# Kernel tuning notes

Measured on AMD Instinct MI355X. Metric: run time of the kernel, lower is better.

Reference implementation:

```python
import jax, jax.numpy as jnp
import numpy as np

TEMPERATURE = 1.0
MAX_ITERS = 10
EPSILON = 1e-4
N, D, K = 131072, 64, 64


def setup_inputs() -> dict:
    key = jax.random.key(0)
    k1, k2 = jax.random.split(key)
    weights = jax.random.normal(k1, (N, D), dtype=jnp.float32)
    init_clusters = jax.random.normal(k2, (K, D), dtype=jnp.float32)
    return {"weights": weights, "init_clusters": init_clusters}


def _dkm(weights, init_clusters):
    n, d = weights.shape
    k = init_clusters.shape[0]
    w_sq = jnp.sum(weights * weights, axis=1, keepdims=True)  # [N,1]

    def step(carry, _):
        clusters, attn_prev, done = carry
        # Euclidean cdist via the expansion ||w||^2 + ||c||^2 - 2 w.c
        c_sq = jnp.sum(clusters * clusters, axis=1)               # [K]
        d2 = w_sq + c_sq[None, :] - 2.0 * (weights @ clusters.T)  # [N,K]
        dist = jnp.sqrt(jnp.maximum(d2, 0.0))
        attn = jax.nn.softmax(-dist / TEMPERATURE, axis=-1)        # [N,K]
        new_clusters = (attn.T @ weights) / jnp.sum(attn, axis=0)[:, None]  # [K,D]
        converged = jnp.linalg.norm(clusters - new_clusters) <= EPSILON
        # Torch breaks BEFORE assigning new_clusters; emulate with a done flag.
        clusters_next = jnp.where(done | converged, clusters, new_clusters)
        attn_next = jnp.where(done, attn_prev, attn)
        return (clusters_next, attn_next, done | converged), None

    init = (init_clusters, jnp.zeros((n, k), weights.dtype), jnp.array(False))
    (clusters, attn, _), _ = jax.lax.scan(step, init, None, length=MAX_ITERS)
    compressed = attn @ clusters  # [N,D]
    return compressed, clusters, attn


def reference(weights, init_clusters):
    return _dkm(weights, init_clusters)
```

## Files before the change

kernel.cpp:

```cpp
#include <hip/hip_runtime.h>
#include <math.h>
#include <stdint.h>

#define N_ROWS 131072
#define DIM 64
#define KC 64
#define NBLK 512
#define ROWS_PB 256

typedef __attribute__((ext_vector_type(8))) short short8;
typedef __attribute__((ext_vector_type(8))) unsigned short ushort8;
typedef __attribute__((ext_vector_type(16))) float float16;
typedef __attribute__((ext_vector_type(2))) unsigned long long ulong2v;

#define PARTIAL_OFF 0u
#define SUMA_OFF    2097152u
#define WSQ_OFF     2129920u
#define NEWC_OFF    2260992u
#define NORM_BYTE_OFF (2265088ull * 4ull)

__device__ __forceinline__ uint32_t rne16(float a) {
  uint32_t u = __float_as_uint(a);
  return (u + 0x7fffu + ((u >> 16) & 1u)) >> 16;
}

__device__ __forceinline__ uint32_t pack_bf16(float a, float b) {
  return rne16(a) | (rne16(b) << 16);
}

__device__ __forceinline__ void split2(float a, float b, uint32_t& hi, uint32_t& lo) {
  uint32_t ha = rne16(a), hb = rne16(b);
  hi = ha | (hb << 16);
  float la = a - __uint_as_float(ha << 16);
  float lb = b - __uint_as_float(hb << 16);
  lo = pack_bf16(la, lb);
}

__global__ __launch_bounds__(256) void prep_kernel(const float* __restrict__ W,
                                                   unsigned short* WS,
                                                   float* __restrict__ wsq) {
  const int t = threadIdx.x;
  const int r = blockIdx.x * 256 + t;
  const float4* p = (const float4*)(W + (size_t)r * DIM);
  uint32_t* hi = (uint32_t*)(WS + (size_t)r * 128);
  uint32_t* lo = hi + 32;
  float s = 0.f;
#pragma unroll
  for (int c = 0; c < 16; ++c) {
    float4 v = p[c];
    s += v.x * v.x + v.y * v.y + v.z * v.z + v.w * v.w;
    uint32_t h0, h1, l0, l1;
    split2(v.x, v.y, h0, l0);
    split2(v.z, v.w, h1, l1);
    hi[c * 2] = h0; hi[c * 2 + 1] = h1;
    lo[c * 2] = l0; lo[c * 2 + 1] = l1;
  }
  wsq[r] = s;
}

__global__ __launch_bounds__(256, 3) void dkm_iter(
    const unsigned short* WS, const float* __restrict__ wsq,
    const float* __restrict__ Cinit,
    const float* __restrict__ newC, float* __restrict__ cur,
    const double* __restrict__ normpart,
    float* __restrict__ partial, float* __restrict__ sumA,
    float* attn_out, int useSel, int writeAttn)
{
  __shared__ __align__(16) short CbfHi[64][68];
  __shared__ __align__(16) short CbfLo[64][68];
  __shared__ __align__(16) short attnT[64][136];
  __shared__ __align__(16) short WTsh[64][136];
  __shared__ float csqL[64];
  __shared__ float wsqL[128];
  __shared__ int s_cond;

  const int t = threadIdx.x;
  const int blk = blockIdx.x;
  const int wid = t >> 6, lane = t & 63, l31 = lane & 31, lh = lane >> 5;
  const int mg = wid >> 1, ng = wid & 1;
  const int rowBase = blk * ROWS_PB;
  const int colA = wid * 32 + l31;

  const unsigned short* pws =
      WS + (size_t)(rowBase + wid * 32 + l31) * 128 + lh * 8;
  ushort8 vh[4], vl[4];
#pragma unroll
  for (int ko = 0; ko < 4; ++ko) {
    vh[ko] = *(const ushort8*)(pws + ko * 16);
    vl[ko] = *(const ushort8*)(pws + 64 + ko * 16);
  }

  if (wid == 0) {
    double v = 0.0;
    if (useSel) {
#pragma unroll
      for (int i = 0; i < 8; ++i) v += normpart[lane + 64 * i];
    }
    v += __shfl_xor(v, 1); v += __shfl_xor(v, 2); v += __shfl_xor(v, 4);
    v += __shfl_xor(v, 8); v += __shfl_xor(v, 16); v += __shfl_xor(v, 32);
    if (lane == 0) s_cond = (v > 1.0e-8) ? 1 : 0;
  }
  __syncthreads();

  const float* src = useSel ? (s_cond ? newC : cur) : Cinit;

  {
    const int crow = t >> 2, cc = (t & 3) * 16;
    float sq = 0.f;
#pragma unroll
    for (int q = 0; q < 4; ++q) {
      float4 c0 = *(const float4*)(src + crow * 64 + cc + q * 4);
      if (blk == 0) *(float4*)(cur + crow * 64 + cc + q * 4) = c0;
      uint32_t h0, h1, l0, l1;
      split2(c0.x, c0.y, h0, l0);
      split2(c0.z, c0.w, h1, l1);
      uint32_t* ph = (uint32_t*)&CbfHi[crow][cc + q * 4];
      ph[0] = h0; ph[1] = h1;
      uint32_t* pl = (uint32_t*)&CbfLo[crow][cc + q * 4];
      pl[0] = l0; pl[1] = l1;
      sq += c0.x*c0.x + c0.y*c0.y + c0.z*c0.z + c0.w*c0.w;
    }
    sq += __shfl_xor(sq, 1);
    sq += __shfl_xor(sq, 2);
    if ((t & 3) == 0) csqL[crow] = sq;
  }
  __syncthreads();

  float16 Uacc = {0,0,0,0, 0,0,0,0, 0,0,0,0, 0,0,0,0};
  float16 Uacc1 = {0,0,0,0, 0,0,0,0, 0,0,0,0, 0,0,0,0};
  const short8 ones = {0x3F80, 0x3F80, 0x3F80, 0x3F80,
                       0x3F80, 0x3F80, 0x3F80, 0x3F80};
  const float cq0 = csqL[l31], cq1 = csqL[32 + l31];

#pragma unroll
  for (int c = 0; c < 2; ++c) {
    const int chunkBase = rowBase + c * 128;

    if (t < 128) wsqL[t] = wsq[chunkBase + t];

    float16 dot0 = {0,0,0,0, 0,0,0,0, 0,0,0,0, 0,0,0,0};
    float16 dot1 = {0,0,0,0, 0,0,0,0, 0,0,0,0, 0,0,0,0};
#pragma unroll
    for (int ko = 0; ko < 4; ++ko) {
      const int d0 = ko * 16 + lh * 8;
      WTsh[d0 + 0][colA] = vh[ko][0];  WTsh[d0 + 1][colA] = vh[ko][1];
      WTsh[d0 + 2][colA] = vh[ko][2];  WTsh[d0 + 3][colA] = vh[ko][3];
      WTsh[d0 + 4][colA] = vh[ko][4];  WTsh[d0 + 5][colA] = vh[ko][5];
      WTsh[d0 + 6][colA] = vh[ko][6];  WTsh[d0 + 7][colA] = vh[ko][7];
      short8 aHi = __builtin_bit_cast(short8, vh[ko]);
      short8 aLo = __builtin_bit_cast(short8, vl[ko]);
#pragma unroll
      for (int nt = 0; nt < 2; ++nt) {
        const unsigned long long* ph = (const unsigned long long*)&CbfHi[nt * 32 + l31][ko * 16 + lh * 8];
        const unsigned long long* pl = (const unsigned long long*)&CbfLo[nt * 32 + l31][ko * 16 + lh * 8];
        ulong2v vhh = {ph[0], ph[1]};
        ulong2v vll = {pl[0], pl[1]};
        short8 cHi = __builtin_bit_cast(short8, vhh);
        short8 cLo = __builtin_bit_cast(short8, vll);
        float16& dd = nt ? dot1 : dot0;
        dd = __builtin_amdgcn_mfma_f32_32x32x16_bf16(aHi, cHi, dd, 0, 0, 0);
        dd = __builtin_amdgcn_mfma_f32_32x32x16_bf16(aLo, cHi, dd, 0, 0, 0);
        dd = __builtin_amdgcn_mfma_f32_32x32x16_bf16(aHi, cLo, dd, 0, 0, 0);
      }
    }

    if (c == 0) {
      const unsigned short* pwN = pws + 128 * 128;
#pragma unroll
      for (int ko = 0; ko < 4; ++ko) {
        vh[ko] = *(const ushort8*)(pwN + ko * 16);
        vl[ko] = *(const ushort8*)(pwN + 64 + ko * 16);
      }
    }

#pragma unroll
    for (int j = 0; j < 16; ++j) {
      const int trow = (j & 3) + 8 * (j >> 2) + 4 * lh;
      const float w2 = wsqL[wid * 32 + trow];
      float g0 = -sqrtf(fmaxf(fmaf(-2.f, dot0[j], w2 + cq0), 0.f));
      float g1 = -sqrtf(fmaxf(fmaf(-2.f, dot1[j], w2 + cq1), 0.f));
      dot0[j] = __expf(g0);
      dot1[j] = __expf(g1);
    }

    if (writeAttn) {
#pragma unroll
      for (int j = 0; j < 16; ++j) {
        const int trow = (j & 3) + 8 * (j >> 2) + 4 * lh;
        float sj = dot0[j] + dot1[j];
        sj += __shfl_xor(sj, 1);  sj += __shfl_xor(sj, 2);  sj += __shfl_xor(sj, 4);
        sj += __shfl_xor(sj, 8);  sj += __shfl_xor(sj, 16);
        float inv = __builtin_amdgcn_rcpf(sj);
        attn_out[(size_t)(chunkBase + wid * 32 + trow) * 64 + l31] = dot0[j] * inv;
        attn_out[(size_t)(chunkBase + wid * 32 + trow) * 64 + 32 + l31] = dot1[j] * inv;
      }
    }

    {
      uint32_t* aT = (uint32_t*)&attnT[0][0];
      const int cb = wid * 16;
#pragma unroll
      for (int h = 0; h < 4; ++h) {
        const int base = cb + 4 * h + 2 * lh;
        aT[l31 * 68 + base]     = pack_bf16(dot0[4 * h],     dot0[4 * h + 1]);
        aT[l31 * 68 + base + 1] = pack_bf16(dot0[4 * h + 2], dot0[4 * h + 3]);
        aT[(32 + l31) * 68 + base]     = pack_bf16(dot1[4 * h],     dot1[4 * h + 1]);
        aT[(32 + l31) * 68 + base + 1] = pack_bf16(dot1[4 * h + 2], dot1[4 * h + 3]);
      }
    }
    __syncthreads();

    float* invsL = wsqL;
    {
      const int r = t >> 1, kh = t & 1;
      float s = 0.f;
#pragma unroll
      for (int kk = 0; kk < 32; ++kk) {
        uint32_t v = (uint32_t)(unsigned short)attnT[kh * 32 + kk][r];
        s += __uint_as_float(v << 16);
      }
      s += __shfl_xor(s, 1);
      if (kh == 0) invsL[r] = __builtin_amdgcn_rcpf(s);
    }
    __syncthreads();

    {
      const int k = t >> 2, q = t & 3;
      uint32_t* row = (uint32_t*)&attnT[k][0];
#pragma unroll
      for (int i = 0; i < 16; ++i) {
        const int ii = (i + k) & 15;
        const int r2 = q * 32 + 2 * ii;
        uint32_t dv = row[q * 16 + ii];
        float lo = __uint_as_float(dv << 16) * invsL[r2];
        float hi = __uint_as_float(dv & 0xffff0000u) * invsL[r2 + 1];
        row[q * 16 + ii] = pack_bf16(lo, hi);
      }
    }
    __syncthreads();

#pragma unroll
    for (int kc = 0; kc < 8; ++kc) {
      const unsigned long long* pa =
          (const unsigned long long*)&attnT[mg * 32 + l31][kc * 16 + lh * 8];
      ulong2v va = {pa[0], pa[1]};
      short8 af = __builtin_bit_cast(short8, va);
      const unsigned long long* pb =
          (const unsigned long long*)&WTsh[ng * 32 + l31][kc * 16 + lh * 8];
      ulong2v vb = {pb[0], pb[1]};
      short8 bf = __builtin_bit_cast(short8, vb);
      Uacc = __builtin_amdgcn_mfma_f32_32x32x16_bf16(af, bf, Uacc, 0, 0, 0);
      Uacc1 = __builtin_amdgcn_mfma_f32_32x32x16_bf16(af, ones, Uacc1, 0, 0, 0);
    }
    __syncthreads();
  }

#pragma unroll
  for (int j = 0; j < 16; ++j) {
    const int k = mg * 32 + (j & 3) + 8 * (j >> 2) + 4 * lh;
    partial[((size_t)blk * 64 + k) * 64 + ng * 32 + l31] = Uacc[j];
  }
  if (ng == 0 && l31 == 0) {
#pragma unroll
    for (int j = 0; j < 16; ++j) {
      const int k = mg * 32 + (j & 3) + 8 * (j >> 2) + 4 * lh;
      sumA[blk * 64 + k] = Uacc1[j];
    }
  }
}

__global__ __launch_bounds__(256) void reduce_kernel(
    const float* __restrict__ partial, const float* __restrict__ sumAp,
    const float* __restrict__ curC, float* __restrict__ newC,
    double* __restrict__ normpart) {
  const int k = blockIdx.x >> 3, oct = blockIdx.x & 7;
  const int t = threadIdx.x;
  const int d = oct * 8 + (t & 7), q = t >> 3;
  double acc = 0.0;
  for (int b = q * 16; b < q * 16 + 16; ++b)
    acc += (double)partial[((size_t)b * 64 + k) * 64 + d];
  __shared__ double sh[256];
  __shared__ double sh2[256];
  sh[t] = acc;
  sh2[t] = (double)sumAp[t * 64 + k] + (double)sumAp[(t + 256) * 64 + k];
  __syncthreads();
#pragma unroll
  for (int s = 128; s >= 8; s >>= 1) {
    if (t < s) { sh[t] += sh[t + s]; sh2[t] += sh2[t + s]; }
    __syncthreads();
  }
#pragma unroll
  for (int s = 4; s >= 1; s >>= 1) {
    if (t < s) sh2[t] += sh2[t + s];
    __syncthreads();
  }
  if (t < 8) {
    float nc = (float)(sh[t] / sh2[0]);
    newC[k * 64 + d] = nc;
    double diff = (double)curC[k * 64 + d] - (double)nc;
    sh[t] = diff * diff;
  }
  __syncthreads();
  if (t == 0) {
    double s = 0.0;
#pragma unroll
    for (int i = 0; i < 8; ++i) s += sh[i];
    normpart[blockIdx.x] = s;
  }
}

__global__ __launch_bounds__(256) void finalize_kernel(
    const double* __restrict__ np, const float* __restrict__ newC,
    const float* __restrict__ cur, float* __restrict__ clusters_out) {
  __shared__ double sh[64];
  __shared__ int sc;
  int t = threadIdx.x;
  if (t < 64) {
    double v = 0.0;
#pragma unroll
    for (int i = 0; i < 8; ++i) v += np[t + 64 * i];
    sh[t] = v;
  }
  __syncthreads();
  if (t == 0) {
    double s = 0.0;
    for (int i = 0; i < 64; ++i) s += sh[i];
    sc = (s > 1.0e-8) ? 1 : 0;
  }
  __syncthreads();
  const float* src = sc ? newC : cur;
  for (int m = t; m < 4096; m += 256) {
    float v = src[m];
    clusters_out[m] = v;
  }
}

__global__ __launch_bounds__(256) void compress_kernel(
    const float* __restrict__ attn, const float* __restrict__ Cl,
    float* __restrict__ outC) {
  __shared__ float Csh[64 * 64];
  __shared__ float Ash[64 * 64];
  float4* Csh4 = (float4*)Csh;
  float4* Ash4 = (float4*)Ash;
  const int t = threadIdx.x;
  const int blk = blockIdx.x;
  const int rowBase = blk * 256;
  const int rg = t >> 4, dg = t & 15;

  {
    const float4* gC = (const float4*)Cl;
#pragma unroll
    for (int q = 0; q < 4; ++q) {
      int m = t + 256 * q;
      Csh4[m ^ ((m >> 6) & 15)] = gC[m];
    }
  }

  for (int tile = 0; tile < 4; ++tile) {
    __syncthreads();
    {
      const float4* gA = (const float4*)(attn + (size_t)(rowBase + tile * 64) * KC);
#pragma unroll
      for (int q = 0; q < 4; ++q) {
        int m = t + 256 * q;
        Ash4[m ^ ((m >> 6) & 15)] = gA[m];
      }
    }
    __syncthreads();
    float acc[4][4] = {{0.f}};
#pragma unroll 4
    for (int c = 0; c < 16; ++c) {
      float4 av[4], cv[4];
#pragma unroll
      for (int i = 0; i < 4; ++i) av[i] = Ash4[((rg * 4 + i) * 16 + c) ^ rg];
#pragma unroll
      for (int j = 0; j < 4; ++j) cv[j] = Csh4[((c * 4 + j) * 16 + dg) ^ c];
#pragma unroll
      for (int i = 0; i < 4; ++i) {
        float a0 = fmaf(av[i].x, cv[0].x, acc[i][0]);
        a0 = fmaf(av[i].y, cv[1].x, a0);
        a0 = fmaf(av[i].z, cv[2].x, a0);
        acc[i][0] = fmaf(av[i].w, cv[3].x, a0);
        float a1 = fmaf(av[i].x, cv[0].y, acc[i][1]);
        a1 = fmaf(av[i].y, cv[1].y, a1);
        a1 = fmaf(av[i].z, cv[2].y, a1);
        acc[i][1] = fmaf(av[i].w, cv[3].y, a1);
        float a2 = fmaf(av[i].x, cv[0].z, acc[i][2]);
        a2 = fmaf(av[i].y, cv[1].z, a2);
        a2 = fmaf(av[i].z, cv[2].z, a2);
        acc[i][2] = fmaf(av[i].w, cv[3].z, a2);
        float a3 = fmaf(av[i].x, cv[0].w, acc[i][3]);
        a3 = fmaf(av[i].y, cv[1].w, a3);
        a3 = fmaf(av[i].z, cv[2].w, a3);
        acc[i][3] = fmaf(av[i].w, cv[3].w, a3);
      }
    }
    float4* gO = (float4*)(outC + (size_t)(rowBase + tile * 64) * DIM);
#pragma unroll
    for (int i = 0; i < 4; ++i)
      gO[(rg * 4 + i) * 16 + dg] = make_float4(acc[i][0], acc[i][1], acc[i][2], acc[i][3]);
  }
}

extern "C" void kernel_launch(void* const* d_in, const int* in_sizes, int n_in,
                              void* d_out, int out_size, void* d_ws, size_t ws_size,
                              hipStream_t stream) {
  (void)in_sizes; (void)n_in; (void)d_ws; (void)ws_size; (void)out_size;
  const float* W = (const float*)d_in[0];
  const float* Cinit = (const float*)d_in[1];
  float* ob = (float*)d_out;

  float* compressed = ob;
  float* clusters_out = ob + (size_t)N_ROWS * DIM;
  float* attn_out = ob + (size_t)N_ROWS * DIM + KC * DIM;

  unsigned short* WS = (unsigned short*)attn_out;
  float* partial = ob + PARTIAL_OFF;
  float* sumAp = ob + SUMA_OFF;
  float* wsq = ob + WSQ_OFF;
  float* newC = ob + NEWC_OFF;
  float* cur = clusters_out;
  double* normpart = (double*)((char*)d_out + NORM_BYTE_OFF);

  prep_kernel<<<NBLK, 256, 0, stream>>>(W, WS, wsq);

  for (int it = 0; it < 10; ++it) {
    dkm_iter<<<NBLK, 256, 0, stream>>>(WS, wsq, Cinit, newC, cur, normpart,
                                       partial, sumAp, attn_out,
                                       (it > 0) ? 1 : 0, (it == 9) ? 1 : 0);
    reduce_kernel<<<512, 256, 0, stream>>>(partial, sumAp, cur, newC, normpart);
  }
  finalize_kernel<<<1, 256, 0, stream>>>(normpart, newC, cur, clusters_out);
  compress_kernel<<<512, 256, 0, stream>>>(attn_out, clusters_out, compressed);
}
```

Baseline: 339.7 us.

## Precompute transposed bf16 weights in prep and read them directly in iteration kernel

```diff
diff --git a/kernel.cpp b/kernel.cpp
--- a/kernel.cpp
+++ b/kernel.cpp
@@ -18,6 +18,7 @@
 #define WSQ_OFF     2129920u
 #define NEWC_OFF    2260992u
 #define NORM_BYTE_OFF (2265088ull * 4ull)
+#define WT_OFF      4194304u
 
 __device__ __forceinline__ uint32_t rne16(float a) {
   uint32_t u = __float_as_uint(a);
@@ -38,9 +39,12 @@
 
 __global__ __launch_bounds__(256) void prep_kernel(const float* __restrict__ W,
                                                    unsigned short* WS,
-                                                   float* __restrict__ wsq) {
+                                                   float* __restrict__ wsq,
+                                                   unsigned short* __restrict__ WT) {
+  __shared__ unsigned short Tsh[64][256];
   const int t = threadIdx.x;
-  const int r = blockIdx.x * 256 + t;
+  const int blk = blockIdx.x;
+  const int r = blk * 256 + t;
   const float4* p = (const float4*)(W + (size_t)r * DIM);
   uint32_t* hi = (uint32_t*)(WS + (size_t)r * 128);
   uint32_t* lo = hi + 32;
@@ -54,12 +58,25 @@
     split2(v.z, v.w, h1, l1);
     hi[c * 2] = h0; hi[c * 2 + 1] = h1;
     lo[c * 2] = l0; lo[c * 2 + 1] = l1;
+    Tsh[c * 4 + 0][t] = (unsigned short)h0;
+    Tsh[c * 4 + 1][t] = (unsigned short)(h0 >> 16);
+    Tsh[c * 4 + 2][t] = (unsigned short)h1;
+    Tsh[c * 4 + 3][t] = (unsigned short)(h1 >> 16);
   }
   wsq[r] = s;
-}
-
-__global__ __launch_bounds__(256, 3) void dkm_iter(
+  __syncthreads();
+#pragma unroll
+  for (int it = 0; it < 8; ++it) {
+    const int idx = it * 256 + t;
+    const int d = idx >> 5, c8 = (idx & 31) * 8;
+    ushort8 v = *(const ushort8*)&Tsh[d][c8];
+    *(ushort8*)(WT + (size_t)d * N_ROWS + blk * 256 + c8) = v;
+  }
+}
+
+__global__ __launch_bounds__(256, 4) void dkm_iter(
     const unsigned short* WS, const float* __restrict__ wsq,
+    const unsigned short* __restrict__ WT,
     const float* __restrict__ Cinit,
     const float* __restrict__ newC, float* __restrict__ cur,
     const double* __restrict__ normpart,
@@ -69,7 +86,6 @@
   __shared__ __align__(16) short CbfHi[64][68];
   __shared__ __align__(16) short CbfLo[64][68];
   __shared__ __align__(16) short attnT[64][136];
-  __shared__ __align__(16) short WTsh[64][136];
   __shared__ float csqL[64];
   __shared__ float wsqL[128];
   __shared__ int s_cond;
@@ -79,7 +95,6 @@
   const int wid = t >> 6, lane = t & 63, l31 = lane & 31, lh = lane >> 5;
   const int mg = wid >> 1, ng = wid & 1;
   const int rowBase = blk * ROWS_PB;
-  const int colA = wid * 32 + l31;
 
   const unsigned short* pws =
       WS + (size_t)(rowBase + wid * 32 + l31) * 128 + lh * 8;
@@ -142,11 +157,6 @@
     float16 dot1 = {0,0,0,0, 0,0,0,0, 0,0,0,0, 0,0,0,0};
 #pragma unroll
     for (int ko = 0; ko < 4; ++ko) {
-      const int d0 = ko * 16 + lh * 8;
-      WTsh[d0 + 0][colA] = vh[ko][0];  WTsh[d0 + 1][colA] = vh[ko][1];
-      WTsh[d0 + 2][colA] = vh[ko][2];  WTsh[d0 + 3][colA] = vh[ko][3];
-      WTsh[d0 + 4][colA] = vh[ko][4];  WTsh[d0 + 5][colA] = vh[ko][5];
-      WTsh[d0 + 6][colA] = vh[ko][6];  WTsh[d0 + 7][colA] = vh[ko][7];
       short8 aHi = __builtin_bit_cast(short8, vh[ko]);
       short8 aLo = __builtin_bit_cast(short8, vl[ko]);
 #pragma unroll
@@ -239,16 +249,16 @@
     }
     __syncthreads();
 
+    const unsigned short* pwt =
+        WT + (size_t)(ng * 32 + l31) * N_ROWS + chunkBase + lh * 8;
 #pragma unroll
     for (int kc = 0; kc < 8; ++kc) {
       const unsigned long long* pa =
           (const unsigned long long*)&attnT[mg * 32 + l31][kc * 16 + lh * 8];
       ulong2v va = {pa[0], pa[1]};
       short8 af = __builtin_bit_cast(short8, va);
-      const unsigned long long* pb =
-          (const unsigned long long*)&WTsh[ng * 32 + l31][kc * 16 + lh * 8];
-      ulong2v vb = {pb[0], pb[1]};
-      short8 bf = __builtin_bit_cast(short8, vb);
+      ushort8 wv = *(const ushort8*)(pwt + kc * 16);
+      short8 bf = __builtin_bit_cast(short8, wv);
       Uacc = __builtin_amdgcn_mfma_f32_32x32x16_bf16(af, bf, Uacc, 0, 0, 0);
       Uacc1 = __builtin_amdgcn_mfma_f32_32x32x16_bf16(af, ones, Uacc1, 0, 0, 0);
     }
@@ -415,6 +425,7 @@
   float* attn_out = ob + (size_t)N_ROWS * DIM + KC * DIM;
 
   unsigned short* WS = (unsigned short*)attn_out;
+  unsigned short* WT = (unsigned short*)(ob + WT_OFF);
   float* partial = ob + PARTIAL_OFF;
   float* sumAp = ob + SUMA_OFF;
   float* wsq = ob + WSQ_OFF;
@@ -422,10 +433,10 @@
   float* cur = clusters_out;
   double* normpart = (double*)((char*)d_out + NORM_BYTE_OFF);
 
-  prep_kernel<<<NBLK, 256, 0, stream>>>(W, WS, wsq);
+  prep_kernel<<<NBLK, 256, 0, stream>>>(W, WS, wsq, WT);
 
   for (int it = 0; it < 10; ++it) {
-    dkm_iter<<<NBLK, 256, 0, stream>>>(WS, wsq, Cinit, newC, cur, normpart,
+    dkm_iter<<<NBLK, 256, 0, stream>>>(WS, wsq, WT, Cinit, newC, cur, normpart,
                                        partial, sumAp, attn_out,
                                        (it > 0) ? 1 : 0, (it == 9) ? 1 : 0);
     reduce_kernel<<<512, 256, 0, stream>>>(partial, sumAp, cur, newC, normpart);
```

New measurement: 441.9 us. +30.1%, slower.
